# Kernel tuning notes

Measured on AMD Instinct MI355X. Metric: run time of the kernel, lower is better.

Reference implementation:

```python
import jax, jax.numpy as jnp
import numpy as np
from jax import lax
from jax.scipy.special import logsumexp

B, T, N = 256, 512, 128


def setup_inputs() -> dict:
    key = jax.random.key(0)
    k1, k2, k3 = jax.random.split(key, 3)
    emissions = jax.random.normal(k1, (B, T, N), dtype=jnp.float32)
    tag_ids = jax.random.randint(k2, (B, T), 0, N, dtype=jnp.int64)
    mask = jnp.ones((B, T), dtype=jnp.int32)
    # learned transition matrix (glorot-uniform-ish init)
    limit = float(np.sqrt(6.0 / (N + N)))
    trans = jax.random.uniform(k3, (N, N), minval=-limit, maxval=limit, dtype=jnp.float32)
    return {"emissions": emissions, "tag_ids": tag_ids, "mask": mask, "trans": trans}


def _sequence_score(emissions, tag_ids, maskf, trans):
    # unary: emission score of the gold tag at each valid step
    unary = jnp.take_along_axis(emissions, tag_ids[:, :, None], axis=2)[..., 0]  # [B,T]
    unary = jnp.sum(unary * maskf, axis=1)
    # binary: transition score between consecutive gold tags
    binary = trans[tag_ids[:, :-1], tag_ids[:, 1:]] * maskf[:, 1:]  # [B,T-1]
    return unary + jnp.sum(binary, axis=1)


def _log_norm(emissions, maskf, trans):
    # forward algorithm over time via lax.scan; alpha: [B,N]
    alpha0 = emissions[:, 0]
    em = jnp.swapaxes(emissions, 0, 1)[1:]   # [T-1,B,N]
    mk = jnp.swapaxes(maskf, 0, 1)[1:]       # [T-1,B]

    def step(alpha, xs):
        emit_t, m_t = xs
        new = logsumexp(alpha[:, :, None] + trans[None], axis=1) + emit_t
        alpha = jnp.where(m_t[:, None] > 0, new, alpha)
        return alpha, None

    alpha, _ = lax.scan(step, alpha0, (em, mk))
    return logsumexp(alpha, axis=1)  # [B]


def _viterbi_decode(emissions, maskf, trans):
    alpha0 = emissions[:, 0]
    em = jnp.swapaxes(emissions, 0, 1)[1:]
    mk = jnp.swapaxes(maskf, 0, 1)[1:]
    idx = jnp.arange(N, dtype=jnp.int32)[None]

    def fwd(alpha, xs):
        emit_t, m_t = xs
        scores = alpha[:, :, None] + trans[None]        # [B,N,N]
        bp = jnp.argmax(scores, axis=1).astype(jnp.int32)  # [B,N]
        new = jnp.max(scores, axis=1) + emit_t
        valid = m_t[:, None] > 0
        alpha = jnp.where(valid, new, alpha)
        bp = jnp.where(valid, bp, idx)  # carry same tag through padding
        return alpha, bp

    alpha, bps = lax.scan(fwd, alpha0, (em, mk))  # bps: [T-1,B,N]
    last_tag = jnp.argmax(alpha, axis=1).astype(jnp.int32)  # [B]

    def bwd(tag, bp_t):
        new_tag = jnp.take_along_axis(bp_t, tag[:, None], axis=1)[:, 0]
        return new_tag, new_tag

    _, tags_rev = lax.scan(bwd, last_tag, bps[::-1])  # [T-1,B]
    tags = jnp.concatenate([tags_rev[::-1], last_tag[None]], axis=0)  # [T,B]
    return jnp.swapaxes(tags, 0, 1)  # [B,T]


def reference(emissions, tag_ids, mask, trans):
    maskf = mask.astype(emissions.dtype)
    log_likelihood = _sequence_score(emissions, tag_ids, maskf, trans) - _log_norm(emissions, maskf, trans)
    predict = _viterbi_decode(emissions, maskf, trans)
    return (log_likelihood, trans, predict)
```

## Files before the change

kernel.cpp:

```cpp
#include <hip/hip_runtime.h>
#include <cmath>

#define BB 256
#define TT 512
#define NN 128
#define LN2F 0.6931471805599453f

typedef __bf16 bf16x8 __attribute__((ext_vector_type(8)));
typedef float floatx4 __attribute__((ext_vector_type(4)));

__device__ __forceinline__ float wave_max64(float v) {
    #pragma unroll
    for (int off = 32; off; off >>= 1) v = fmaxf(v, __shfl_xor(v, off));
    return v;
}
__device__ __forceinline__ float wave_sum64(float v) {
    #pragma unroll
    for (int off = 32; off; off >>= 1) v += __shfl_xor(v, off);
    return v;
}
__device__ __forceinline__ int wave_argmax128(float v0, float v1, int l) {
    float m = fmaxf(v0, v1);
    float wm = wave_max64(m);
    unsigned long long ball = __ballot(m == wm);
    int lane = __ffsll(ball) - 1;
    int idx = (v0 == wm) ? (2 * l) : (2 * l + 1);
    return __shfl(idx, lane);
}

__device__ __forceinline__ __bf16 to_bf16(float f) {
    unsigned u = __float_as_uint(f);
    unsigned r = (u + 0x7FFFu + ((u >> 16) & 1u)) >> 16;
    union { unsigned short s; __bf16 b; } cv;
    cv.s = (unsigned short)r;
    return cv.b;
}

__device__ __forceinline__ int padidx(int i) { return 36 * (i >> 5) + (i & 31); }

__global__ __launch_bounds__(512, 4) void fwd_kernel(
        const float* __restrict__ em, const int* __restrict__ mask,
        const float* __restrict__ trans, float* __restrict__ outp,
        float* __restrict__ lognorm) {
    const int bi = blockIdx.x;
    const bool isV = bi < BB;
    const int b = isV ? bi : bi - BB;
    const int tid = threadIdx.x;
    const int w = tid >> 6;
    const int l = tid & 63;
    const int j = (l & 15) + 16 * w;
    const int q = l >> 4;
    const int i0 = 32 * q;

    __shared__ __align__(16) float stA[144], stB[144];
    __shared__ __align__(16) __bf16 sbf[2][NN];
    __shared__ unsigned char bp_lds[TT * NN];
    __shared__ unsigned char tags_lds[TT];
    __shared__ unsigned char map_lds[8 * NN];
    __shared__ int entry_sh[8];
    __shared__ int msk[TT];
    __shared__ float piv[2];
    __shared__ float sfin[NN];
    __shared__ int misc[2];

    msk[tid] = mask[b * TT + tid];

    const float* emb = em + (size_t)b * TT * NN;

    if (isV) {
        float C[32];
        {
            const float* tc = trans + (size_t)i0 * NN + j;
            #pragma unroll
            for (int r = 0; r < 32; ++r) C[r] = tc[(size_t)r * NN];
        }
        float st = 0.f;
        {
            float a0 = emb[j];
            st = a0;
            if (l < 16) stA[padidx(j)] = a0;
        }
        float e_next = emb[NN + j];
        __syncthreads();

        const float4* apA = (const float4*)(stA + 36 * q);
        const float4* apB = (const float4*)(stB + 36 * q);

        auto VSTEP = [&](int t, const float4* ap, float* dst) {
            const float e_cur = e_next;
            if (t + 1 < TT) e_next = emb[(size_t)(t + 1) * NN + j];
            const int m = msk[t];
            float m0 = -INFINITY, m1 = -INFINITY, m2 = -INFINITY, m3 = -INFINITY;
            int u0 = 0, u1 = 0, u2 = 0, u3 = 0;
            #pragma unroll
            for (int u = 0; u < 8; ++u) {
                float4 v = ap[u];
                float c0 = v.x + C[4*u+0]; u0 = (c0 > m0) ? u : u0; m0 = fmaxf(m0, c0);
                float c1 = v.y + C[4*u+1]; u1 = (c1 > m1) ? u : u1; m1 = fmaxf(m1, c1);
                float c2 = v.z + C[4*u+2]; u2 = (c2 > m2) ? u : u2; m2 = fmaxf(m2, c2);
                float c3 = v.w + C[4*u+3]; u3 = (c3 > m3) ? u : u3; m3 = fmaxf(m3, c3);
            }
            float bv = m0; int bx = i0 + 4 * u0;
            { int id = i0 + 4*u1 + 1; if (m1 > bv || (m1 == bv && id < bx)) { bv = m1; bx = id; } }
            { int id = i0 + 4*u2 + 2; if (m2 > bv || (m2 == bv && id < bx)) { bv = m2; bx = id; } }
            { int id = i0 + 4*u3 + 3; if (m3 > bv || (m3 == bv && id < bx)) { bv = m3; bx = id; } }
            #pragma unroll
            for (int off = 16; off <= 32; off <<= 1) {
                float ov = __shfl_xor(bv, off);
                int oi = __shfl_xor(bx, off);
                if (ov > bv || (ov == bv && oi < bx)) { bv = ov; bx = oi; }
            }
            if (l < 16) {
                float an; int bp;
                if (m) { an = bv + e_cur; bp = bx; }
                else   { an = st;         bp = j;  }
                st = an;
                dst[padidx(j)] = an;
                bp_lds[t * NN + j] = (unsigned char)bp;
            }
            __syncthreads();
        };

        for (int t = 1; t < TT - 1; t += 2) {
            VSTEP(t, apA, stB);
            VSTEP(t + 1, apB, stA);
        }
        VSTEP(TT - 1, apA, stB);

        if (w == 0) {
            float a0 = stB[padidx(2 * l)], a1 = stB[padidx(2 * l + 1)];
            int tg = wave_argmax128(a0, a1, l);
            if (l == 0) { misc[0] = tg; tags_lds[TT - 1] = (unsigned char)tg; }
        }
        __syncthreads();
        const int lo = 64 * w + 1;
        const int hi = (w == 7) ? (TT - 1) : (64 * w + 64);
        {
            int tA = 2 * l, tB = 2 * l + 1;
            for (int t = hi; t >= lo; --t) {
                tA = bp_lds[t * NN + tA];
                tB = bp_lds[t * NN + tB];
            }
            map_lds[w * NN + 2 * l]     = (unsigned char)tA;
            map_lds[w * NN + 2 * l + 1] = (unsigned char)tB;
        }
        __syncthreads();
        if (tid == 0) {
            int e = misc[0];
            entry_sh[7] = e;
            for (int c = 7; c >= 1; --c) { e = map_lds[c * NN + e]; entry_sh[c - 1] = e; }
        }
        __syncthreads();
        if (l == 0) {
            int tg = entry_sh[w];
            for (int t = hi; t >= lo; --t) {
                tg = bp_lds[t * NN + tg];
                tags_lds[t - 1] = (unsigned char)tg;
            }
        }
        __syncthreads();
        outp[(size_t)b * TT + tid] = (float)tags_lds[tid];
    } else {
        bf16x8 Bf[4];
        #pragma unroll
        for (int kc = 0; kc < 4; ++kc) {
            #pragma unroll
            for (int jj = 0; jj < 8; ++jj) {
                int row = kc * 32 + q * 8 + jj;
                Bf[kc][jj] = to_bf16(__expf(trans[(size_t)row * NN + j]));
            }
        }
        float ss = __expf(emb[j]);
        int kacc = 0;
        if (l < 16) sbf[0][j] = to_bf16(ss);
        if (tid == 0) piv[0] = ss;
        float e_next = emb[NN + j];
        __syncthreads();

        for (int t = 1; t < TT; ++t) {
            const float e_cur = e_next;
            if (t + 1 < TT) e_next = emb[(size_t)(t + 1) * NN + j];
            const int m = msk[t];
            const int p = (t - 1) & 1, qb = t & 1;
            if (m) {
                const __bf16* sp = sbf[p];
                floatx4 acc = {0.f, 0.f, 0.f, 0.f};
                #pragma unroll
                for (int kc = 0; kc < 4; ++kc) {
                    bf16x8 a = *(const bf16x8*)(sp + kc * 32 + q * 8);
                    acc = __builtin_amdgcn_mfma_f32_16x16x32_bf16(a, Bf[kc], acc, 0, 0, 0);
                }
                float dot = acc[0];
                const float pv = piv[p];
                const int k = (int)(__float_as_uint(pv) >> 23) - 127;
                const float scale = __uint_as_float((unsigned)(127 - k) << 23);
                ss = dot * scale * __expf(e_cur);
                if (tid == 0) kacc += k;
            }
            if (l < 16) sbf[qb][j] = to_bf16(ss);
            if (tid == 0) piv[qb] = ss;
            __syncthreads();
        }

        if (l < 16) sfin[j] = ss;
        if (tid == 0) misc[1] = kacc;
        __syncthreads();
        if (w == 0) {
            float v = sfin[2 * l] + sfin[2 * l + 1];
            v = wave_sum64(v);
            if (l == 0) lognorm[b] = __logf(v) + (float)misc[1] * LN2F;
        }
    }
}

__global__ __launch_bounds__(128, 1) void score_kernel(
        const float* __restrict__ em, const int* __restrict__ tags,
        const int* __restrict__ mask, const float* __restrict__ trans,
        const float* __restrict__ lognorm, float* __restrict__ out_ll) {
    const int b = blockIdx.x;
    const int tid = threadIdx.x;
    float acc = 0.f;
    for (int t = tid; t < TT; t += 128) {
        int tg = tags[b * TT + t];
        float mf = (float)mask[b * TT + t];
        acc += em[((size_t)b * TT + t) * NN + tg] * mf;
        if (t >= 1) {
            int tp = tags[b * TT + t - 1];
            acc += trans[tp * NN + tg] * mf;
        }
    }
    acc = wave_sum64(acc);
    __shared__ float rs[2];
    if ((tid & 63) == 0) rs[tid >> 6] = acc;
    __syncthreads();
    if (tid == 0) out_ll[b] = (rs[0] + rs[1]) - lognorm[b];
}

__global__ void copy_trans_kernel(const float* __restrict__ trans,
                                  float* __restrict__ dst) {
    int i = blockIdx.x * 256 + threadIdx.x;
    if (i < NN * NN) dst[i] = trans[i];
}

extern "C" void kernel_launch(void* const* d_in, const int* in_sizes, int n_in,
                              void* d_out, int out_size, void* d_ws, size_t ws_size,
                              hipStream_t stream) {
    const float* em = (const float*)d_in[0];
    const int* tags = (const int*)d_in[1];
    const int* mask = (const int*)d_in[2];
    const float* trans = (const float*)d_in[3];

    float* out = (float*)d_out;
    float* out_ll = out;
    float* out_trans = out + BB;
    float* out_pred = out + BB + NN * NN;

    float* lognorm = (float*)d_ws;

    hipLaunchKernelGGL(fwd_kernel, dim3(2 * BB), dim3(512), 0, stream,
                       em, mask, trans, out_pred, lognorm);
    hipLaunchKernelGGL(copy_trans_kernel, dim3(64), dim3(256), 0, stream,
                       trans, out_trans);
    hipLaunchKernelGGL(score_kernel, dim3(BB), dim3(128), 0, stream,
                       em, tags, mask, trans, lognorm, out_ll);
}
```

Before: 539.9 us.

## Fuse Viterbi, forward-algorithm, score and copy into one 1024-thread kernel

Replaces the three-kernel launch (split Viterbi/logsumexp blocks, a separate score kernel, a trans copy) with one kernel per batch element. Each block runs Viterbi on 16 waves, each handling 8 tags with 16-wide partial max, while 8 of those waves also run the MFMA-based forward recursion in the same time step. One barrier per step now serves both recursions. Backtrace is split into 16 chunks, and gold-path scoring and the trans copy happen at the end. This removes extra launches and the lognorm round-trip through global memory and halves the per-thread Viterbi work. The cost is 1024-thread blocks with heavier per-step work, which may limit occupancy, and both recursions now serialise on the same barrier.

```diff
diff --git a/kernel.cpp b/kernel.cpp
--- a/kernel.cpp
+++ b/kernel.cpp
@@ -36,217 +36,210 @@
     return cv.b;
 }
 
-__device__ __forceinline__ int padidx(int i) { return 36 * (i >> 5) + (i & 31); }
-
-__global__ __launch_bounds__(512, 4) void fwd_kernel(
-        const float* __restrict__ em, const int* __restrict__ mask,
-        const float* __restrict__ trans, float* __restrict__ outp,
-        float* __restrict__ lognorm) {
-    const int bi = blockIdx.x;
-    const bool isV = bi < BB;
-    const int b = isV ? bi : bi - BB;
+__device__ __forceinline__ int padidx16(int i) { return 20 * (i >> 4) + (i & 15); }
+
+__global__ __launch_bounds__(1024, 4) void fused_kernel(
+        const float* __restrict__ em, const int* __restrict__ gtags,
+        const int* __restrict__ mask, const float* __restrict__ trans,
+        float* __restrict__ out_ll, float* __restrict__ out_trans,
+        float* __restrict__ outp) {
+    const int b = blockIdx.x;
     const int tid = threadIdx.x;
     const int w = tid >> 6;
     const int l = tid & 63;
-    const int j = (l & 15) + 16 * w;
-    const int q = l >> 4;
-    const int i0 = 32 * q;
-
-    __shared__ __align__(16) float stA[144], stB[144];
+    const int jv = (l & 7) + 8 * w;
+    const int q = l >> 3;
+    const int i0 = 16 * q;
+    const bool sAct = (w < 8);
+    const int js = (l & 15) + 16 * (w & 7);
+    const int qs = l >> 4;
+
+    __shared__ __align__(16) float stA[1440], stB[1440];
     __shared__ __align__(16) __bf16 sbf[2][NN];
     __shared__ unsigned char bp_lds[TT * NN];
     __shared__ unsigned char tags_lds[TT];
-    __shared__ unsigned char map_lds[8 * NN];
-    __shared__ int entry_sh[8];
+    __shared__ unsigned char map_lds[16 * NN];
+    __shared__ int entry_sh[16];
     __shared__ int msk[TT];
     __shared__ float piv[2];
     __shared__ float sfin[NN];
+    __shared__ float wsum[16];
+    __shared__ float llnorm_sh;
     __shared__ int misc[2];
 
-    msk[tid] = mask[b * TT + tid];
+    if (tid < TT) msk[tid] = mask[b * TT + tid];
 
     const float* emb = em + (size_t)b * TT * NN;
 
-    if (isV) {
-        float C[32];
-        {
-            const float* tc = trans + (size_t)i0 * NN + j;
-            #pragma unroll
-            for (int r = 0; r < 32; ++r) C[r] = tc[(size_t)r * NN];
-        }
-        float st = 0.f;
-        {
-            float a0 = emb[j];
-            st = a0;
-            if (l < 16) stA[padidx(j)] = a0;
-        }
-        float e_next = emb[NN + j];
-        __syncthreads();
-
-        const float4* apA = (const float4*)(stA + 36 * q);
-        const float4* apB = (const float4*)(stB + 36 * q);
-
-        auto VSTEP = [&](int t, const float4* ap, float* dst) {
-            const float e_cur = e_next;
-            if (t + 1 < TT) e_next = emb[(size_t)(t + 1) * NN + j];
-            const int m = msk[t];
-            float m0 = -INFINITY, m1 = -INFINITY, m2 = -INFINITY, m3 = -INFINITY;
-            int u0 = 0, u1 = 0, u2 = 0, u3 = 0;
-            #pragma unroll
-            for (int u = 0; u < 8; ++u) {
-                float4 v = ap[u];
-                float c0 = v.x + C[4*u+0]; u0 = (c0 > m0) ? u : u0; m0 = fmaxf(m0, c0);
-                float c1 = v.y + C[4*u+1]; u1 = (c1 > m1) ? u : u1; m1 = fmaxf(m1, c1);
-                float c2 = v.z + C[4*u+2]; u2 = (c2 > m2) ? u : u2; m2 = fmaxf(m2, c2);
-                float c3 = v.w + C[4*u+3]; u3 = (c3 > m3) ? u : u3; m3 = fmaxf(m3, c3);
-            }
-            float bv = m0; int bx = i0 + 4 * u0;
-            { int id = i0 + 4*u1 + 1; if (m1 > bv || (m1 == bv && id < bx)) { bv = m1; bx = id; } }
-            { int id = i0 + 4*u2 + 2; if (m2 > bv || (m2 == bv && id < bx)) { bv = m2; bx = id; } }
-            { int id = i0 + 4*u3 + 3; if (m3 > bv || (m3 == bv && id < bx)) { bv = m3; bx = id; } }
-            #pragma unroll
-            for (int off = 16; off <= 32; off <<= 1) {
-                float ov = __shfl_xor(bv, off);
-                int oi = __shfl_xor(bx, off);
-                if (ov > bv || (ov == bv && oi < bx)) { bv = ov; bx = oi; }
-            }
-            if (l < 16) {
-                float an; int bp;
-                if (m) { an = bv + e_cur; bp = bx; }
-                else   { an = st;         bp = j;  }
-                st = an;
-                dst[padidx(j)] = an;
-                bp_lds[t * NN + j] = (unsigned char)bp;
-            }
-            __syncthreads();
-        };
-
-        for (int t = 1; t < TT - 1; t += 2) {
-            VSTEP(t, apA, stB);
-            VSTEP(t + 1, apB, stA);
-        }
-        VSTEP(TT - 1, apA, stB);
-
-        if (w == 0) {
-            float a0 = stB[padidx(2 * l)], a1 = stB[padidx(2 * l + 1)];
-            int tg = wave_argmax128(a0, a1, l);
-            if (l == 0) { misc[0] = tg; tags_lds[TT - 1] = (unsigned char)tg; }
-        }
-        __syncthreads();
-        const int lo = 64 * w + 1;
-        const int hi = (w == 7) ? (TT - 1) : (64 * w + 64);
-        {
-            int tA = 2 * l, tB = 2 * l + 1;
-            for (int t = hi; t >= lo; --t) {
-                tA = bp_lds[t * NN + tA];
-                tB = bp_lds[t * NN + tB];
-            }
-            map_lds[w * NN + 2 * l]     = (unsigned char)tA;
-            map_lds[w * NN + 2 * l + 1] = (unsigned char)tB;
-        }
-        __syncthreads();
-        if (tid == 0) {
-            int e = misc[0];
-            entry_sh[7] = e;
-            for (int c = 7; c >= 1; --c) { e = map_lds[c * NN + e]; entry_sh[c - 1] = e; }
-        }
-        __syncthreads();
-        if (l == 0) {
-            int tg = entry_sh[w];
-            for (int t = hi; t >= lo; --t) {
-                tg = bp_lds[t * NN + tg];
-                tags_lds[t - 1] = (unsigned char)tg;
-            }
-        }
-        __syncthreads();
-        outp[(size_t)b * TT + tid] = (float)tags_lds[tid];
-    } else {
-        bf16x8 Bf[4];
+    float C[16];
+    {
+        const float* tc = trans + (size_t)i0 * NN + jv;
+        #pragma unroll
+        for (int r = 0; r < 16; ++r) C[r] = tc[(size_t)r * NN];
+    }
+    float st;
+    {
+        float a0 = emb[jv];
+        st = a0;
+        if (l < 8) stA[padidx16(jv)] = a0;
+    }
+    float e_next = emb[NN + jv];
+
+    bf16x8 Bf[4];
+    float ss = 0.f, es_next = 0.f;
+    int kacc = 0;
+    if (sAct) {
         #pragma unroll
         for (int kc = 0; kc < 4; ++kc) {
             #pragma unroll
             for (int jj = 0; jj < 8; ++jj) {
-                int row = kc * 32 + q * 8 + jj;
-                Bf[kc][jj] = to_bf16(__expf(trans[(size_t)row * NN + j]));
+                int row = kc * 32 + qs * 8 + jj;
+                Bf[kc][jj] = to_bf16(__expf(trans[(size_t)row * NN + js]));
             }
         }
-        float ss = __expf(emb[j]);
-        int kacc = 0;
-        if (l < 16) sbf[0][j] = to_bf16(ss);
+        ss = __expf(emb[js]);
+        if (l < 16) sbf[0][js] = to_bf16(ss);
         if (tid == 0) piv[0] = ss;
-        float e_next = emb[NN + j];
-        __syncthreads();
-
-        for (int t = 1; t < TT; ++t) {
-            const float e_cur = e_next;
-            if (t + 1 < TT) e_next = emb[(size_t)(t + 1) * NN + j];
-            const int m = msk[t];
-            const int p = (t - 1) & 1, qb = t & 1;
+        es_next = emb[NN + js];
+    }
+    __syncthreads();
+
+    const float4* apA = (const float4*)(stA + 20 * q);
+    const float4* apB = (const float4*)(stB + 20 * q);
+
+    auto STEP = [&](int t, const float4* ap, float* dst) {
+        const float e_cur = e_next;
+        const float es_cur = es_next;
+        if (t + 1 < TT) {
+            e_next = emb[(size_t)(t + 1) * NN + jv];
+            if (sAct) es_next = emb[(size_t)(t + 1) * NN + js];
+        }
+        const int m = msk[t];
+        float m0 = -INFINITY, m1 = -INFINITY, m2 = -INFINITY, m3 = -INFINITY;
+        int u0 = 0, u1 = 0, u2 = 0, u3 = 0;
+        #pragma unroll
+        for (int u = 0; u < 4; ++u) {
+            float4 v = ap[u];
+            float c0 = v.x + C[4*u+0]; u0 = (c0 > m0) ? u : u0; m0 = fmaxf(m0, c0);
+            float c1 = v.y + C[4*u+1]; u1 = (c1 > m1) ? u : u1; m1 = fmaxf(m1, c1);
+            float c2 = v.z + C[4*u+2]; u2 = (c2 > m2) ? u : u2; m2 = fmaxf(m2, c2);
+            float c3 = v.w + C[4*u+3]; u3 = (c3 > m3) ? u : u3; m3 = fmaxf(m3, c3);
+        }
+        float bv = m0; int bx = i0 + 4 * u0;
+        { int id = i0 + 4*u1 + 1; if (m1 > bv || (m1 == bv && id < bx)) { bv = m1; bx = id; } }
+        { int id = i0 + 4*u2 + 2; if (m2 > bv || (m2 == bv && id < bx)) { bv = m2; bx = id; } }
+        { int id = i0 + 4*u3 + 3; if (m3 > bv || (m3 == bv && id < bx)) { bv = m3; bx = id; } }
+        #pragma unroll
+        for (int off = 8; off <= 32; off <<= 1) {
+            float ov = __shfl_xor(bv, off);
+            int oi = __shfl_xor(bx, off);
+            if (ov > bv || (ov == bv && oi < bx)) { bv = ov; bx = oi; }
+        }
+        if (l < 8) {
+            float an; int bp;
+            if (m) { an = bv + e_cur; bp = bx; }
+            else   { an = st;         bp = jv; }
+            st = an;
+            dst[padidx16(jv)] = an;
+            bp_lds[t * NN + jv] = (unsigned char)bp;
+        }
+        if (sAct) {
             if (m) {
+                const int p = (t - 1) & 1;
                 const __bf16* sp = sbf[p];
                 floatx4 acc = {0.f, 0.f, 0.f, 0.f};
                 #pragma unroll
                 for (int kc = 0; kc < 4; ++kc) {
-                    bf16x8 a = *(const bf16x8*)(sp + kc * 32 + q * 8);
+                    bf16x8 a = *(const bf16x8*)(sp + kc * 32 + qs * 8);
                     acc = __builtin_amdgcn_mfma_f32_16x16x32_bf16(a, Bf[kc], acc, 0, 0, 0);
                 }
                 float dot = acc[0];
                 const float pv = piv[p];
                 const int k = (int)(__float_as_uint(pv) >> 23) - 127;
                 const float scale = __uint_as_float((unsigned)(127 - k) << 23);
-                ss = dot * scale * __expf(e_cur);
+                ss = dot * scale * __expf(es_cur);
                 if (tid == 0) kacc += k;
             }
-            if (l < 16) sbf[qb][j] = to_bf16(ss);
+            const int qb = t & 1;
+            if (l < 16) sbf[qb][js] = to_bf16(ss);
             if (tid == 0) piv[qb] = ss;
-            __syncthreads();
-        }
-
-        if (l < 16) sfin[j] = ss;
-        if (tid == 0) misc[1] = kacc;
+        }
         __syncthreads();
-        if (w == 0) {
-            float v = sfin[2 * l] + sfin[2 * l + 1];
-            v = wave_sum64(v);
-            if (l == 0) lognorm[b] = __logf(v) + (float)misc[1] * LN2F;
-        }
-    }
-}
-
-__global__ __launch_bounds__(128, 1) void score_kernel(
-        const float* __restrict__ em, const int* __restrict__ tags,
-        const int* __restrict__ mask, const float* __restrict__ trans,
-        const float* __restrict__ lognorm, float* __restrict__ out_ll) {
-    const int b = blockIdx.x;
-    const int tid = threadIdx.x;
+    };
+
+    for (int t = 1; t < TT - 1; t += 2) {
+        STEP(t, apA, stB);
+        STEP(t + 1, apB, stA);
+    }
+    STEP(TT - 1, apA, stB);
+
+    if (sAct && l < 16) sfin[js] = ss;
+    if (tid == 0) misc[1] = kacc;
+    if (w == 0) {
+        float a0 = stB[padidx16(2 * l)], a1 = stB[padidx16(2 * l + 1)];
+        int tg = wave_argmax128(a0, a1, l);
+        if (l == 0) { misc[0] = tg; tags_lds[TT - 1] = (unsigned char)tg; }
+    }
+    if (tid < 64) out_trans[b * 64 + tid] = trans[b * 64 + tid];
+    __syncthreads();
+    if (w == 1) {
+        float v = sfin[2 * l] + sfin[2 * l + 1];
+        v = wave_sum64(v);
+        if (l == 0) llnorm_sh = __logf(v) + (float)misc[1] * LN2F;
+    }
+    const int lo = 32 * w + 1;
+    const int hi = (w == 15) ? (TT - 1) : (32 * w + 32);
+    {
+        int tA = 2 * l, tB = 2 * l + 1;
+        for (int t = hi; t >= lo; --t) {
+            tA = bp_lds[t * NN + tA];
+            tB = bp_lds[t * NN + tB];
+        }
+        map_lds[w * NN + 2 * l]     = (unsigned char)tA;
+        map_lds[w * NN + 2 * l + 1] = (unsigned char)tB;
+    }
+    __syncthreads();
+    if (tid == 0) {
+        int e = misc[0];
+        entry_sh[15] = e;
+        for (int c = 15; c >= 1; --c) { e = map_lds[c * NN + e]; entry_sh[c - 1] = e; }
+    }
+    __syncthreads();
+    if (l == 0) {
+        int tg = entry_sh[w];
+        for (int t = hi; t >= lo; --t) {
+            tg = bp_lds[t * NN + tg];
+            tags_lds[t - 1] = (unsigned char)tg;
+        }
+    }
+    __syncthreads();
     float acc = 0.f;
-    for (int t = tid; t < TT; t += 128) {
-        int tg = tags[b * TT + t];
-        float mf = (float)mask[b * TT + t];
-        acc += em[((size_t)b * TT + t) * NN + tg] * mf;
-        if (t >= 1) {
-            int tp = tags[b * TT + t - 1];
+    if (tid < TT) {
+        outp[(size_t)b * TT + tid] = (float)tags_lds[tid];
+        int tg = gtags[b * TT + tid];
+        float mf = (float)msk[tid];
+        acc = emb[(size_t)tid * NN + tg] * mf;
+        if (tid >= 1) {
+            int tp = gtags[b * TT + tid - 1];
             acc += trans[tp * NN + tg] * mf;
         }
     }
     acc = wave_sum64(acc);
-    __shared__ float rs[2];
-    if ((tid & 63) == 0) rs[tid >> 6] = acc;
-    __syncthreads();
-    if (tid == 0) out_ll[b] = (rs[0] + rs[1]) - lognorm[b];
-}
-
-__global__ void copy_trans_kernel(const float* __restrict__ trans,
-                                  float* __restrict__ dst) {
-    int i = blockIdx.x * 256 + threadIdx.x;
-    if (i < NN * NN) dst[i] = trans[i];
+    if (l == 0) wsum[w] = acc;
+    __syncthreads();
+    if (tid == 0) {
+        float s = 0.f;
+        #pragma unroll
+        for (int i = 0; i < 16; ++i) s += wsum[i];
+        out_ll[b] = s - llnorm_sh;
+    }
 }
 
 extern "C" void kernel_launch(void* const* d_in, const int* in_sizes, int n_in,
                               void* d_out, int out_size, void* d_ws, size_t ws_size,
                               hipStream_t stream) {
     const float* em = (const float*)d_in[0];
-    const int* tags = (const int*)d_in[1];
+    const int* gtags = (const int*)d_in[1];
     const int* mask = (const int*)d_in[2];
     const float* trans = (const float*)d_in[3];
 
@@ -255,12 +248,6 @@
     float* out_trans = out + BB;
     float* out_pred = out + BB + NN * NN;
 
-    float* lognorm = (float*)d_ws;
-
-    hipLaunchKernelGGL(fwd_kernel, dim3(2 * BB), dim3(512), 0, stream,
-                       em, mask, trans, out_pred, lognorm);
-    hipLaunchKernelGGL(copy_trans_kernel, dim3(64), dim3(256), 0, stream,
-                       trans, out_trans);
-    hipLaunchKernelGGL(score_kernel, dim3(BB), dim3(128), 0, stream,
-                       em, tags, mask, trans, lognorm, out_ll);
-}
+    hipLaunchKernelGGL(fused_kernel, dim3(BB), dim3(1024), 0, stream,
+                       em, gtags, mask, trans, out_ll, out_trans, out_pred);
+}
```

Result: slower. 623.5 us (+15.5%).

## Fuse score and trans-copy kernels into forward kernel; batch LDS loads in Viterbi step

Applied to the files above, without the earlier changes.

The gold-sequence score computation and the transition-matrix copy move into the existing fused forward/Viterbi kernel, which removes two extra kernel launches and the lognorm round-trip through workspace memory. The score is computed per sequence by the log-norm blocks, and each Viterbi block copies a 64-element slice of trans. The Viterbi step also loads all eight float4 alpha values from LDS before doing the max/argmax chain, so the reads can be issued together. The cost is some extra tail work inside the long-running fused kernel and more register pressure in the step loop.

```diff
diff --git a/kernel.cpp b/kernel.cpp
--- a/kernel.cpp
+++ b/kernel.cpp
@@ -39,9 +39,10 @@
 __device__ __forceinline__ int padidx(int i) { return 36 * (i >> 5) + (i & 31); }
 
 __global__ __launch_bounds__(512, 4) void fwd_kernel(
-        const float* __restrict__ em, const int* __restrict__ mask,
-        const float* __restrict__ trans, float* __restrict__ outp,
-        float* __restrict__ lognorm) {
+        const float* __restrict__ em, const int* __restrict__ gtags,
+        const int* __restrict__ mask, const float* __restrict__ trans,
+        float* __restrict__ out_ll, float* __restrict__ out_trans,
+        float* __restrict__ outp) {
     const int bi = blockIdx.x;
     const bool isV = bi < BB;
     const int b = isV ? bi : bi - BB;
@@ -61,6 +62,8 @@
     __shared__ int msk[TT];
     __shared__ float piv[2];
     __shared__ float sfin[NN];
+    __shared__ float wsum[8];
+    __shared__ float llnorm_sh;
     __shared__ int misc[2];
 
     msk[tid] = mask[b * TT + tid];
@@ -90,15 +93,17 @@
             const float e_cur = e_next;
             if (t + 1 < TT) e_next = emb[(size_t)(t + 1) * NN + j];
             const int m = msk[t];
+            float4 vv[8];
+            #pragma unroll
+            for (int u = 0; u < 8; ++u) vv[u] = ap[u];
             float m0 = -INFINITY, m1 = -INFINITY, m2 = -INFINITY, m3 = -INFINITY;
             int u0 = 0, u1 = 0, u2 = 0, u3 = 0;
             #pragma unroll
             for (int u = 0; u < 8; ++u) {
-                float4 v = ap[u];
-                float c0 = v.x + C[4*u+0]; u0 = (c0 > m0) ? u : u0; m0 = fmaxf(m0, c0);
-                float c1 = v.y + C[4*u+1]; u1 = (c1 > m1) ? u : u1; m1 = fmaxf(m1, c1);
-                float c2 = v.z + C[4*u+2]; u2 = (c2 > m2) ? u : u2; m2 = fmaxf(m2, c2);
-                float c3 = v.w + C[4*u+3]; u3 = (c3 > m3) ? u : u3; m3 = fmaxf(m3, c3);
+                float c0 = vv[u].x + C[4*u+0]; u0 = (c0 > m0) ? u : u0; m0 = fmaxf(m0, c0);
+                float c1 = vv[u].y + C[4*u+1]; u1 = (c1 > m1) ? u : u1; m1 = fmaxf(m1, c1);
+                float c2 = vv[u].z + C[4*u+2]; u2 = (c2 > m2) ? u : u2; m2 = fmaxf(m2, c2);
+                float c3 = vv[u].w + C[4*u+3]; u3 = (c3 > m3) ? u : u3; m3 = fmaxf(m3, c3);
             }
             float bv = m0; int bx = i0 + 4 * u0;
             { int id = i0 + 4*u1 + 1; if (m1 > bv || (m1 == bv && id < bx)) { bv = m1; bx = id; } }
@@ -132,6 +137,7 @@
             int tg = wave_argmax128(a0, a1, l);
             if (l == 0) { misc[0] = tg; tags_lds[TT - 1] = (unsigned char)tg; }
         }
+        if (tid < 64) out_trans[b * 64 + tid] = trans[b * 64 + tid];
         __syncthreads();
         const int lo = 64 * w + 1;
         const int hi = (w == 7) ? (TT - 1) : (64 * w + 64);
@@ -208,45 +214,35 @@
         if (w == 0) {
             float v = sfin[2 * l] + sfin[2 * l + 1];
             v = wave_sum64(v);
-            if (l == 0) lognorm[b] = __logf(v) + (float)misc[1] * LN2F;
+            if (l == 0) llnorm_sh = __logf(v) + (float)misc[1] * LN2F;
+        }
+        float acc = 0.f;
+        {
+            int tg = gtags[b * TT + tid];
+            float mf = (float)msk[tid];
+            acc = emb[(size_t)tid * NN + tg] * mf;
+            if (tid >= 1) {
+                int tp = gtags[b * TT + tid - 1];
+                acc += trans[tp * NN + tg] * mf;
+            }
+        }
+        acc = wave_sum64(acc);
+        if (l == 0) wsum[w] = acc;
+        __syncthreads();
+        if (tid == 0) {
+            float s = 0.f;
+            #pragma unroll
+            for (int i = 0; i < 8; ++i) s += wsum[i];
+            out_ll[b] = s - llnorm_sh;
         }
     }
-}
-
-__global__ __launch_bounds__(128, 1) void score_kernel(
-        const float* __restrict__ em, const int* __restrict__ tags,
-        const int* __restrict__ mask, const float* __restrict__ trans,
-        const float* __restrict__ lognorm, float* __restrict__ out_ll) {
-    const int b = blockIdx.x;
-    const int tid = threadIdx.x;
-    float acc = 0.f;
-    for (int t = tid; t < TT; t += 128) {
-        int tg = tags[b * TT + t];
-        float mf = (float)mask[b * TT + t];
-        acc += em[((size_t)b * TT + t) * NN + tg] * mf;
-        if (t >= 1) {
-            int tp = tags[b * TT + t - 1];
-            acc += trans[tp * NN + tg] * mf;
-        }
-    }
-    acc = wave_sum64(acc);
-    __shared__ float rs[2];
-    if ((tid & 63) == 0) rs[tid >> 6] = acc;
-    __syncthreads();
-    if (tid == 0) out_ll[b] = (rs[0] + rs[1]) - lognorm[b];
-}
-
-__global__ void copy_trans_kernel(const float* __restrict__ trans,
-                                  float* __restrict__ dst) {
-    int i = blockIdx.x * 256 + threadIdx.x;
-    if (i < NN * NN) dst[i] = trans[i];
 }
 
 extern "C" void kernel_launch(void* const* d_in, const int* in_sizes, int n_in,
                               void* d_out, int out_size, void* d_ws, size_t ws_size,
                               hipStream_t stream) {
     const float* em = (const float*)d_in[0];
-    const int* tags = (const int*)d_in[1];
+    const int* gtags = (const int*)d_in[1];
     const int* mask = (const int*)d_in[2];
     const float* trans = (const float*)d_in[3];
 
@@ -255,12 +251,6 @@
     float* out_trans = out + BB;
     float* out_pred = out + BB + NN * NN;
 
-    float* lognorm = (float*)d_ws;
-
     hipLaunchKernelGGL(fwd_kernel, dim3(2 * BB), dim3(512), 0, stream,
-                       em, mask, trans, out_pred, lognorm);
-    hipLaunchKernelGGL(copy_trans_kernel, dim3(64), dim3(256), 0, stream,
-                       trans, out_trans);
-    hipLaunchKernelGGL(score_kernel, dim3(BB), dim3(128), 0, stream,
-                       em, tags, mask, trans, lognorm, out_ll);
-}
+                       em, gtags, mask, trans, out_ll, out_trans, out_pred);
+}
```

Result: faster. 524.8 us (-2.8%).
